# Kernel optimization log

Hardware: AMD Instinct MI355X
Metric: run time of the kernel (lower is better)

Reference implementation:

```python
import jax, jax.numpy as jnp
import numpy as np

B, N, DIN, DOUT, D, C = 64, 8192, 64, 64, 10, 4
NPC = N // C  # nodes per client


def setup_inputs() -> dict:
    key = jax.random.key(0)
    ks = jax.random.split(key, 6)
    x = jax.random.normal(ks[0], (B, N, DIN), dtype=jnp.float32)
    node_embeddings = jax.random.normal(ks[1], (N, D), dtype=jnp.float32)
    poly_coefficients = jax.random.normal(ks[2], (C, 1, 4), dtype=jnp.float32)  # unused in sprtrelu mode
    mask = jnp.ones((B, N, 1), dtype=jnp.float32)
    weights_pool = jax.random.normal(ks[3], (C, D, DIN, DOUT), dtype=jnp.float32)
    bias_pool = jax.random.normal(ks[4], (C, D, DOUT), dtype=jnp.float32)
    nodes_per = jnp.arange(N, dtype=jnp.int64 if jax.config.x64_enabled else jnp.int32).reshape(C, NPC)
    return {"x": x, "node_embeddings": node_embeddings, "poly_coefficients": poly_coefficients,
            "mask": mask, "weights_pool": weights_pool, "bias_pool": bias_pool, "nodes_per": nodes_per}


def reference(x, node_embeddings, poly_coefficients, mask, weights_pool, bias_pool, nodes_per):
    # active_mode='sprtrelu', inter_dropout=0.0 -> bernoulli mask is all ones,
    # so sum_EH is the sum of EH over ALL clients, identical for every client.
    c, n = nodes_per.shape
    b = x.shape[0]
    x = x * mask                                       # [B,N,Din]
    E = node_embeddings[nodes_per]                     # [C,n,D] client-wise gather
    xg = jnp.take(x, nodes_per.reshape(-1), axis=1).reshape(b, c, n, -1)  # [B,C,n,Din]
    tE = jax.nn.relu(E)                                # [C,n,D]
    # per-client EH_c = einsum('nd,bnc->bdc'); sum over clients (bernoulli all ones)
    sum_EH = jnp.einsum('cnd,bcni->bdi', tE, xg)       # [B,D,Din]
    # Z_c = H_c + transformed_E_c @ sum_EH
    Z = xg + jnp.einsum('cnd,bdi->bcni', tE, sum_EH)   # [B,C,n,Din]
    # dynamic per-node weights/bias from embeddings
    W = jnp.einsum('cnd,cdio->cnio', E, weights_pool)  # [C,n,Din,Dout]
    bb = jnp.einsum('cnd,cdo->cno', E, bias_pool)      # [C,n,Dout]
    out = jnp.einsum('bcni,cnio->bcno', Z, W) + bb     # [B,C,n,Dout]
    return out.reshape(b, c * n, -1)                   # concat over clients along node dim
```

## Files before the change

### kernel.cpp

```cpp
#include <hip/hip_runtime.h>
#include <hip/hip_bf16.h>


#define BB 64
#define NN 8192
#define DD 10

typedef __bf16 bf16;
typedef __bf16 bf16x8 __attribute__((ext_vector_type(8)));
typedef float f32x4 __attribute__((ext_vector_type(4)));

__global__ __launch_bounds__(256, 2) void k_sumEH(
    const float* __restrict__ x, const float* __restrict__ emb,
    const float* __restrict__ mask, const int* __restrict__ np,
    float* __restrict__ sEH) {
  __shared__ __align__(16) float red[4][DD][64];

  const int b = blockIdx.x >> 4;
  const int chunk = blockIdx.x & 15;
  const int tid = threadIdx.x;
  const int lane = tid & 63;
  const int w = tid >> 6;
  const int qq = lane >> 4, r16 = lane & 15;

  const f32x4* x4 = (const f32x4*)(x + (size_t)b * NN * 64);
  const float* mb = mask + (size_t)b * NN;
  const int* npb = np + chunk * 512 + w * 128;

  f32x4 acc[DD];
#pragma unroll
  for (int d = 0; d < DD; ++d) acc[d] = (f32x4)0.f;

#pragma unroll 2
  for (int g = 0; g < 32; ++g) {
    const int idx = npb[g * 4 + qq];
    f32x4 xv = x4[(size_t)idx * 16 + r16];
    const float m = mb[idx];
    const float2* e2 = (const float2*)(emb + (size_t)idx * DD);
    const float2 e0 = e2[0], e1 = e2[1], e4 = e2[2], e6 = e2[3], e8 = e2[4];
    xv *= m;
    acc[0] += xv * fmaxf(e0.x, 0.f);
    acc[1] += xv * fmaxf(e0.y, 0.f);
    acc[2] += xv * fmaxf(e1.x, 0.f);
    acc[3] += xv * fmaxf(e1.y, 0.f);
    acc[4] += xv * fmaxf(e4.x, 0.f);
    acc[5] += xv * fmaxf(e4.y, 0.f);
    acc[6] += xv * fmaxf(e6.x, 0.f);
    acc[7] += xv * fmaxf(e6.y, 0.f);
    acc[8] += xv * fmaxf(e8.x, 0.f);
    acc[9] += xv * fmaxf(e8.y, 0.f);
  }

#pragma unroll
  for (int d = 0; d < DD; ++d) {
    f32x4 a = acc[d];
#pragma unroll
    for (int j = 0; j < 4; ++j) {
      float v = a[j];
      v += __shfl_xor(v, 16);
      v += __shfl_xor(v, 32);
      a[j] = v;
    }
    acc[d] = a;
  }
  if (qq == 0) {
#pragma unroll
    for (int d = 0; d < DD; ++d) *(f32x4*)&red[w][d][r16 * 4] = acc[d];
  }
  __syncthreads();

  for (int s = tid; s < DD * 64; s += 256) {
    const int d = s >> 6, i = s & 63;
    const float v = red[0][d][i] + red[1][d][i] + red[2][d][i] + red[3][d][i];
    atomicAdd(sEH + ((size_t)b * DD + d) * 64 + i, v);
  }
}

__global__ __launch_bounds__(256, 2) void k_main(
    const float* __restrict__ x, const float* __restrict__ emb,
    const float* __restrict__ mask, const float* __restrict__ wp,
    const float* __restrict__ bp, const int* __restrict__ np,
    const float* __restrict__ sEH, float* __restrict__ out) {
  __shared__ float E_l[4][DD];
  __shared__ float bb_l[4][64];
  __shared__ float mask_l[64][4];
  __shared__ __align__(16) bf16 Wt[4][64][72];

  const int tid = threadIdx.x;
  const int lane = tid & 63;
  const int w = tid >> 6;
  const int p0 = blockIdx.x * 4;
  const int c = p0 >> 11;

  {
    const int bq = tid >> 2, g = tid & 3;
    mask_l[bq][g] = mask[(size_t)bq * NN + np[p0 + g]];
  }
  if (tid < 40) {
    const int g = tid / 10, d = tid % 10;
    E_l[g][d] = emb[(size_t)np[p0 + g] * DD + d];
  }
  __syncthreads();

  {
    f32x4 accW[16];
#pragma unroll
    for (int p = 0; p < 16; ++p) accW[p] = (f32x4)0.f;
#pragma unroll
    for (int d = 0; d < DD; ++d) {
      f32x4 ev;
      ev[0] = E_l[0][d]; ev[1] = E_l[1][d]; ev[2] = E_l[2][d]; ev[3] = E_l[3][d];
      const float* base = wp + ((size_t)(c * DD + d) * 64 + w * 16) * 64 + lane;
#pragma unroll
      for (int p = 0; p < 16; ++p) accW[p] += ev * base[(size_t)p * 64];
    }
#pragma unroll
    for (int g = 0; g < 4; ++g) {
      bf16x8 v0, v1;
#pragma unroll
      for (int p = 0; p < 8; ++p) { v0[p] = (bf16)accW[p][g]; v1[p] = (bf16)accW[p + 8][g]; }
      *(bf16x8*)&Wt[g][lane][w * 16] = v0;
      *(bf16x8*)&Wt[g][lane][w * 16 + 8] = v1;
    }
    float bacc = 0.f;
#pragma unroll
    for (int d = 0; d < DD; ++d)
      bacc = fmaf(E_l[w][d], bp[((size_t)(c * DD + d)) * 64 + lane], bacc);
    bb_l[w][lane] = bacc;
  }
  __syncthreads();

  const int mynode = np[p0 + w];
  const int q = lane >> 4, r16 = lane & 15;

  bf16x8 wfrag[4][2];
#pragma unroll
  for (int nt = 0; nt < 4; ++nt)
#pragma unroll
    for (int kt = 0; kt < 2; ++kt)
      wfrag[nt][kt] = *(const bf16x8*)&Wt[w][nt * 16 + r16][kt * 32 + q * 8];

  float biasv[4];
#pragma unroll
  for (int nt = 0; nt < 4; ++nt) biasv[nt] = bb_l[w][nt * 16 + r16];

  float tEr[DD];
#pragma unroll
  for (int d = 0; d < DD; ++d) tEr[d] = fmaxf(E_l[w][d], 0.f);

  const f32x4* x4 = (const f32x4*)x;
  const f32x4* s4 = (const f32x4*)sEH;

#pragma unroll
  for (int chunk = 0; chunk < 4; ++chunk) {
    const int b = chunk * 16 + r16;
    const float m = mask_l[b][w];
    const size_t xrow = ((size_t)b * NN + mynode) * 16;
    f32x4 z00 = x4[xrow + q * 2 + 0] * m;
    f32x4 z01 = x4[xrow + q * 2 + 1] * m;
    f32x4 z10 = x4[xrow + 8 + q * 2 + 0] * m;
    f32x4 z11 = x4[xrow + 8 + q * 2 + 1] * m;
    const f32x4* sb = s4 + (size_t)b * DD * 16 + q * 2;
#pragma unroll
    for (int d = 0; d < DD; ++d) {
      const f32x4 s0 = sb[d * 16 + 0];
      const f32x4 s1 = sb[d * 16 + 1];
      const f32x4 s2 = sb[d * 16 + 8];
      const f32x4 s3 = sb[d * 16 + 9];
      const float t = tEr[d];
      z00 += s0 * t;
      z01 += s1 * t;
      z10 += s2 * t;
      z11 += s3 * t;
    }
    bf16x8 a0, a1;
#pragma unroll
    for (int j = 0; j < 4; ++j) {
      a0[j] = (bf16)z00[j];
      a0[4 + j] = (bf16)z01[j];
      a1[j] = (bf16)z10[j];
      a1[4 + j] = (bf16)z11[j];
    }
    f32x4 acc[4];
#pragma unroll
    for (int nt = 0; nt < 4; ++nt) {
      acc[nt][0] = biasv[nt]; acc[nt][1] = biasv[nt];
      acc[nt][2] = biasv[nt]; acc[nt][3] = biasv[nt];
    }
#pragma unroll
    for (int nt = 0; nt < 4; ++nt) {
      acc[nt] = __builtin_amdgcn_mfma_f32_16x16x32_bf16(a0, wfrag[nt][0], acc[nt], 0, 0, 0);
      acc[nt] = __builtin_amdgcn_mfma_f32_16x16x32_bf16(a1, wfrag[nt][1], acc[nt], 0, 0, 0);
    }
    const size_t pg = (size_t)(p0 + w);
#pragma unroll
    for (int nt = 0; nt < 4; ++nt) {
#pragma unroll
      for (int r = 0; r < 4; ++r) {
        const int bg = chunk * 16 + q * 4 + r;
        out[((size_t)bg * NN + pg) * 64 + nt * 16 + r16] = acc[nt][r];
      }
    }
  }
}

extern "C" void kernel_launch(void* const* d_in, const int* in_sizes, int n_in,
                              void* d_out, int out_size, void* d_ws, size_t ws_size,
                              hipStream_t stream) {
  const float* x    = (const float*)d_in[0];
  const float* emb  = (const float*)d_in[1];
  const float* mask = (const float*)d_in[3];
  const float* wp   = (const float*)d_in[4];
  const float* bp   = (const float*)d_in[5];
  const int*   np   = (const int*)d_in[6];
  float* out = (float*)d_out;
  float* sEH = (float*)d_ws;

  hipMemsetAsync(sEH, 0, (size_t)BB * DD * 64 * sizeof(float), stream);
  k_sumEH<<<dim3(BB * 16), dim3(256), 0, stream>>>(x, emb, mask, np, sEH);
  k_main<<<dim3(NN / 4), dim3(256), 0, stream>>>(x, emb, mask, wp, bp, np, sEH, out);
}
```

Baseline: 414.2 us.

## Drop node-index gather in sumEH, stage relu(E)*mask in LDS, prefetch x

```diff
diff --git a/kernel.cpp b/kernel.cpp
--- a/kernel.cpp
+++ b/kernel.cpp
@@ -10,10 +10,11 @@
 typedef __bf16 bf16x8 __attribute__((ext_vector_type(8)));
 typedef float f32x4 __attribute__((ext_vector_type(4)));
 
-__global__ __launch_bounds__(256, 2) void k_sumEH(
+__global__ __launch_bounds__(256, 4) void k_sumEH(
     const float* __restrict__ x, const float* __restrict__ emb,
-    const float* __restrict__ mask, const int* __restrict__ np,
-    float* __restrict__ sEH) {
+    const float* __restrict__ mask, float* __restrict__ sEH) {
+  __shared__ float m_l[512];
+  __shared__ float tEm[512][DD];
   __shared__ __align__(16) float red[4][DD][64];
 
   const int b = blockIdx.x >> 4;
@@ -21,34 +22,37 @@
   const int tid = threadIdx.x;
   const int lane = tid & 63;
   const int w = tid >> 6;
-  const int qq = lane >> 4, r16 = lane & 15;
-
-  const f32x4* x4 = (const f32x4*)(x + (size_t)b * NN * 64);
-  const float* mb = mask + (size_t)b * NN;
-  const int* npb = np + chunk * 512 + w * 128;
+  const int node0 = chunk * 512;
+
+  for (int s = tid; s < 512; s += 256) m_l[s] = mask[(size_t)b * NN + node0 + s];
+  __syncthreads();
+  for (int s = tid; s < 512 * DD; s += 256) {
+    const int nl = s / DD, d = s - nl * DD;
+    tEm[nl][d] = fmaxf(emb[(size_t)node0 * DD + s], 0.f) * m_l[nl];
+  }
+  __syncthreads();
+
+  const int nsub = lane >> 4, r16 = lane & 15;
+  const f32x4* xb4 = (const f32x4*)(x + ((size_t)b * NN + node0 + w * 128) * 64);
 
   f32x4 acc[DD];
 #pragma unroll
   for (int d = 0; d < DD; ++d) acc[d] = (f32x4)0.f;
 
-#pragma unroll 2
+#pragma unroll 4
   for (int g = 0; g < 32; ++g) {
-    const int idx = npb[g * 4 + qq];
-    f32x4 xv = x4[(size_t)idx * 16 + r16];
-    const float m = mb[idx];
-    const float2* e2 = (const float2*)(emb + (size_t)idx * DD);
-    const float2 e0 = e2[0], e1 = e2[1], e4 = e2[2], e6 = e2[3], e8 = e2[4];
-    xv *= m;
-    acc[0] += xv * fmaxf(e0.x, 0.f);
-    acc[1] += xv * fmaxf(e0.y, 0.f);
-    acc[2] += xv * fmaxf(e1.x, 0.f);
-    acc[3] += xv * fmaxf(e1.y, 0.f);
-    acc[4] += xv * fmaxf(e4.x, 0.f);
-    acc[5] += xv * fmaxf(e4.y, 0.f);
-    acc[6] += xv * fmaxf(e6.x, 0.f);
-    acc[7] += xv * fmaxf(e6.y, 0.f);
-    acc[8] += xv * fmaxf(e8.x, 0.f);
-    acc[9] += xv * fmaxf(e8.y, 0.f);
+    const f32x4 xv = xb4[g * 64 + lane];
+    const int nl = w * 128 + g * 4 + nsub;
+    const float2 t01 = *(const float2*)&tEm[nl][0];
+    const float2 t23 = *(const float2*)&tEm[nl][2];
+    const float2 t45 = *(const float2*)&tEm[nl][4];
+    const float2 t67 = *(const float2*)&tEm[nl][6];
+    const float2 t89 = *(const float2*)&tEm[nl][8];
+    acc[0] += xv * t01.x; acc[1] += xv * t01.y;
+    acc[2] += xv * t23.x; acc[3] += xv * t23.y;
+    acc[4] += xv * t45.x; acc[5] += xv * t45.y;
+    acc[6] += xv * t67.x; acc[7] += xv * t67.y;
+    acc[8] += xv * t89.x; acc[9] += xv * t89.y;
   }
 
 #pragma unroll
@@ -63,7 +67,7 @@
     }
     acc[d] = a;
   }
-  if (qq == 0) {
+  if (nsub == 0) {
 #pragma unroll
     for (int d = 0; d < DD; ++d) *(f32x4*)&red[w][d][r16 * 4] = acc[d];
   }
@@ -76,7 +80,7 @@
   }
 }
 
-__global__ __launch_bounds__(256, 2) void k_main(
+__global__ __launch_bounds__(256, 4) void k_main(
     const float* __restrict__ x, const float* __restrict__ emb,
     const float* __restrict__ mask, const float* __restrict__ wp,
     const float* __restrict__ bp, const int* __restrict__ np,
@@ -132,6 +136,19 @@
 
   const int mynode = np[p0 + w];
   const int q = lane >> 4, r16 = lane & 15;
+  const f32x4* x4 = (const f32x4*)x;
+  const f32x4* s4 = (const f32x4*)sEH;
+
+  f32x4 xpre[2][4];
+  auto load_x = [&](int chunk, f32x4* dst) {
+    const int b = chunk * 16 + r16;
+    const size_t xrow = ((size_t)b * NN + mynode) * 16;
+    dst[0] = x4[xrow + q * 2 + 0];
+    dst[1] = x4[xrow + q * 2 + 1];
+    dst[2] = x4[xrow + 8 + q * 2 + 0];
+    dst[3] = x4[xrow + 8 + q * 2 + 1];
+  };
+  load_x(0, xpre[0]);
 
   bf16x8 wfrag[4][2];
 #pragma unroll
@@ -148,18 +165,16 @@
 #pragma unroll
   for (int d = 0; d < DD; ++d) tEr[d] = fmaxf(E_l[w][d], 0.f);
 
-  const f32x4* x4 = (const f32x4*)x;
-  const f32x4* s4 = (const f32x4*)sEH;
-
 #pragma unroll
   for (int chunk = 0; chunk < 4; ++chunk) {
+    if (chunk < 3) load_x(chunk + 1, xpre[(chunk + 1) & 1]);
+    const f32x4* xa = xpre[chunk & 1];
     const int b = chunk * 16 + r16;
     const float m = mask_l[b][w];
-    const size_t xrow = ((size_t)b * NN + mynode) * 16;
-    f32x4 z00 = x4[xrow + q * 2 + 0] * m;
-    f32x4 z01 = x4[xrow + q * 2 + 1] * m;
-    f32x4 z10 = x4[xrow + 8 + q * 2 + 0] * m;
-    f32x4 z11 = x4[xrow + 8 + q * 2 + 1] * m;
+    f32x4 z00 = xa[0] * m;
+    f32x4 z01 = xa[1] * m;
+    f32x4 z10 = xa[2] * m;
+    f32x4 z11 = xa[3] * m;
     const f32x4* sb = s4 + (size_t)b * DD * 16 + q * 2;
 #pragma unroll
     for (int d = 0; d < DD; ++d) {
@@ -217,6 +232,6 @@
   float* sEH = (float*)d_ws;
 
   hipMemsetAsync(sEH, 0, (size_t)BB * DD * 64 * sizeof(float), stream);
-  k_sumEH<<<dim3(BB * 16), dim3(256), 0, stream>>>(x, emb, mask, np, sEH);
+  k_sumEH<<<dim3(BB * 16), dim3(256), 0, stream>>>(x, emb, mask, sEH);
   k_main<<<dim3(NN / 4), dim3(256), 0, stream>>>(x, emb, mask, wp, bp, np, sEH, out);
 }
```

Result: slower. 449.8 us (+8.6%).
